# Kernel optimization log

Hardware: AMD Instinct MI355X
Metric: run time of the kernel (lower is better)

Reference implementation:

```python
import jax, jax.numpy as jnp
import numpy as np

C = 64        # channels
D = 64        # dense grid side at tensor_stride 1
N = 100000    # active voxels


def _conv3d(x, w, stride, pad):
    # x: (D,D,D,Cin), w: (kd,kh,kw,Cin,Cout) -> (D',D',D',Cout)
    return jax.lax.conv_general_dilated(
        x[None], w, window_strides=(stride,) * 3, padding=pad,
        dimension_numbers=('NDHWC', 'DHWIO', 'NDHWC'))[0]


def _sconv(x, w, b, mask, stride=1, pad='SAME'):
    # Minkowski sparse conv == dense conv on zero-filled grid, restricted to
    # the active output sites (bias only added at active sites).
    return (_conv3d(x, w, stride, pad) + b) * mask


def _forward(coords, coords_ds, feats_c1, feats_ref, w_fuse, b_fuse, w_down, b_down,
             w_conv2, b_conv2, w_p00, b_p00, w_p01, b_p01, w_p10, b_p10,
             w_p11, b_p11, w_p12, b_p12):
    dt = feats_c1.dtype
    Dh = D // 2
    ci, cj, ck = coords[:, 0], coords[:, 1], coords[:, 2]
    di, dj, dk = coords_ds[:, 0], coords_ds[:, 1], coords_ds[:, 2]
    mask = jnp.zeros((D, D, D, 1), dt).at[ci, cj, ck, 0].set(1.0)
    mask_ds = jnp.zeros((Dh, Dh, Dh, 1), dt).at[di, dj, dk, 0].set(1.0)
    fused = jnp.concatenate([feats_c1, feats_ref], axis=1)            # (N, 2C)
    x = jnp.zeros((D, D, D, 2 * C), dt).at[ci, cj, ck].set(fused)
    x = jax.nn.relu(_sconv(x, w_fuse, b_fuse, mask))                  # conv_fuse, k=3 s=1
    x = jax.nn.relu(_sconv(x, w_down, b_down, mask_ds, stride=2, pad='VALID'))  # conv_down1, k=2 s=2
    x = _sconv(x, w_conv2, b_conv2, mask_ds)                          # conv_2, no relu
    for i in range(w_p00.shape[0]):                                   # InceptionResNet x3
        p0 = jax.nn.relu(_sconv(x, w_p00[i], b_p00[i], mask_ds))      # k3 C->C/4
        p0 = _sconv(p0, w_p01[i], b_p01[i], mask_ds)                  # k3 C/4->C/2
        p1 = jax.nn.relu(_sconv(x, w_p10[i], b_p10[i], mask_ds))      # k1 C->C/4
        p1 = jax.nn.relu(_sconv(p1, w_p11[i], b_p11[i], mask_ds))     # k3 C/4->C/4
        p1 = _sconv(p1, w_p12[i], b_p12[i], mask_ds)                  # k1 C/4->C/2
        x = jnp.concatenate([p0, p1], axis=-1) + x                    # cat + residual
    return x[di, dj, dk]                                              # (M, C) sparse output feats


def setup_inputs() -> dict:
    rng = np.random.default_rng(0)
    flat = rng.choice(D ** 3, size=N, replace=False)                  # unique occupied voxels
    coords = np.stack(np.unravel_index(flat, (D, D, D)), axis=1).astype(np.int32)
    coords_ds = np.unique(coords // 2, axis=0).astype(np.int32)       # stride-2 active set
    key = jax.random.key(0)
    ks = iter(jax.random.split(key, 40))

    def W(shape, fan_in):
        return jax.random.normal(next(ks), shape, jnp.float32) / np.float32(np.sqrt(fan_in))

    def B(shape):
        return jax.random.normal(next(ks), shape, jnp.float32) * 0.01

    L = 3  # res blocks
    return dict(
        coords=jnp.asarray(coords), coords_ds=jnp.asarray(coords_ds),
        feats_c1=jax.random.normal(next(ks), (N, C), jnp.float32),
        feats_ref=jax.random.normal(next(ks), (N, C), jnp.float32),
        w_fuse=W((3, 3, 3, 2 * C, C), 27 * 2 * C), b_fuse=B((C,)),
        w_down=W((2, 2, 2, C, C), 8 * C), b_down=B((C,)),
        w_conv2=W((3, 3, 3, C, C), 27 * C), b_conv2=B((C,)),
        w_p00=W((L, 3, 3, 3, C, C // 4), 27 * C), b_p00=B((L, C // 4)),
        w_p01=W((L, 3, 3, 3, C // 4, C // 2), 27 * C // 4), b_p01=B((L, C // 2)),
        w_p10=W((L, 1, 1, 1, C, C // 4), C), b_p10=B((L, C // 4)),
        w_p11=W((L, 3, 3, 3, C // 4, C // 4), 27 * C // 4), b_p11=B((L, C // 4)),
        w_p12=W((L, 1, 1, 1, C // 4, C // 2), C // 4), b_p12=B((L, C // 2)),
    )


def reference(coords, coords_ds, feats_c1, feats_ref, w_fuse, b_fuse, w_down, b_down,
              w_conv2, b_conv2, w_p00, b_p00, w_p01, b_p01, w_p10, b_p10,
              w_p11, b_p11, w_p12, b_p12):
    return _forward(coords, coords_ds, feats_c1, feats_ref, w_fuse, b_fuse, w_down,
                    b_down, w_conv2, b_conv2, w_p00, b_p00, w_p01, b_p01, w_p10,
                    b_p10, w_p11, b_p11, w_p12, b_p12)
```

## Files before the change

### kernel.cpp

```cpp
#include <hip/hip_runtime.h>

#define GD 64
#define GDS 32

typedef _Float16 f16;
typedef __attribute__((ext_vector_type(8))) _Float16 f16x8;
typedef __attribute__((ext_vector_type(4))) float f32x4;

#define GLOAD_LDS16(SRC, DST)                                                        \
    __builtin_amdgcn_global_load_lds(                                                \
        (const __attribute__((address_space(1))) unsigned int*)(const void*)(SRC),   \
        (__attribute__((address_space(3))) unsigned int*)(void*)(DST), 16, 0, 0)

__global__ __launch_bounds__(256) void init_pack_kernel(
    int* __restrict__ idx_grid, unsigned char* __restrict__ ds_mask, f16* __restrict__ zrow,
    f16* __restrict__ f1z, const float* __restrict__ wf, const float* __restrict__ wd,
    const float* __restrict__ wc2, const float* __restrict__ wp00, const float* __restrict__ wp01,
    const float* __restrict__ wp10, const float* __restrict__ wp11, const float* __restrict__ wp12,
    const float* __restrict__ bp00, const float* __restrict__ bp01, const float* __restrict__ bp10,
    const float* __restrict__ bp11, int L, f16* __restrict__ wc1, f16* __restrict__ wdnh,
    f16* __restrict__ wc2h, f16* __restrict__ wfA, f16* __restrict__ wfB, f16* __restrict__ w12h,
    float* __restrict__ bA, float* __restrict__ bB) {
    int i0 = blockIdx.x * 256 + threadIdx.x;
    if (i0 < GD * GD * GD) idx_grid[i0] = -1;
    if (i0 < GDS * GDS * GDS) ds_mask[i0] = 0;
    if (i0 < 128) zrow[i0] = (f16)0.f;
    if (i0 < 64) f1z[i0] = (f16)0.f;

    int i = i0;
    int n;
    n = 27 * 8192;
    if (i < n) {
        int tap = i >> 13, oc = (i >> 7) & 63, ic = i & 127;
        wc1[i] = (f16)wf[(tap * 128 + ic) * 64 + oc];
        return;
    }
    i -= n;
    n = 8 * 4096;
    if (i < n) {
        int t = i >> 12, oc = (i >> 6) & 63, ic = i & 63;
        wdnh[i] = (f16)wd[(t * 64 + ic) * 64 + oc];
        return;
    }
    i -= n;
    n = 27 * 4096;
    if (i < n) {
        int tap = i >> 12, oc = (i >> 6) & 63, ic = i & 63;
        wc2h[i] = (f16)wc2[(tap * 64 + ic) * 64 + oc];
        return;
    }
    i -= n;
    n = L * 27 * 2048;
    if (i < n) {
        int l = i / (27 * 2048), r = i - l * 27 * 2048;
        int tap = r >> 11, oc = (r >> 6) & 31, ic = r & 63;
        float v = 0.f;
        if (oc < 16) v = wp00[(((size_t)l * 27 + tap) * 64 + ic) * 16 + oc];
        else if (tap == 13) v = wp10[((size_t)l * 64 + ic) * 16 + (oc - 16)];
        wfA[i] = (f16)v;
        return;
    }
    i -= n;
    n = L * 27 * 1536;
    if (i < n) {
        int l = i / (27 * 1536), r = i - l * 27 * 1536;
        int tap = r / 1536, q = r - tap * 1536;
        int oc = q >> 5, ic = q & 31;
        float v = 0.f;
        if (oc < 32) {
            if (ic < 16) v = wp01[(((size_t)l * 27 + tap) * 16 + ic) * 32 + oc];
        } else {
            if (ic >= 16) v = wp11[(((size_t)l * 27 + tap) * 16 + (ic - 16)) * 16 + (oc - 32)];
        }
        wfB[i] = (f16)v;
        return;
    }
    i -= n;
    n = L * 512;
    if (i < n) {
        int l = i >> 9, q = i & 511, oc = q >> 4, ic = q & 15;
        w12h[i] = (f16)wp12[((size_t)l * 16 + ic) * 32 + oc];
        return;
    }
    i -= n;
    n = L * 32;
    if (i < n) {
        int l = i >> 5, oc = i & 31;
        bA[i] = (oc < 16) ? bp00[l * 16 + oc] : bp10[l * 16 + oc - 16];
        return;
    }
    i -= n;
    n = L * 48;
    if (i < n) {
        int l = i / 48, c = i - l * 48;
        bB[i] = (c < 32) ? bp01[l * 32 + c] : bp11[l * 16 + (c - 32)];
    }
}

__global__ __launch_bounds__(256) void scatter_kernel(const int* __restrict__ coords, int N,
                                                      const int* __restrict__ coords_ds, int M,
                                                      int* __restrict__ idx_grid,
                                                      unsigned char* __restrict__ ds_mask) {
    int i = blockIdx.x * 256 + threadIdx.x;
    if (i < N) {
        int a = coords[i * 3], b = coords[i * 3 + 1], c = coords[i * 3 + 2];
        idx_grid[(a * GD + b) * GD + c] = i;
    }
    if (i < M) {
        int a = coords_ds[i * 3], b = coords_ds[i * 3 + 1], c = coords_ds[i * 3 + 2];
        ds_mask[(a * GDS + b) * GDS + c] = 1;
    }
}

__global__ __launch_bounds__(256) void count_kernel(const int* __restrict__ idx_grid,
                                                    int* __restrict__ cnt) {
    __shared__ int c;
    if (threadIdx.x == 0) c = 0;
    __syncthreads();
    int s = blockIdx.x * 256 + threadIdx.x;
    bool act = idx_grid[s] >= 0;
    unsigned long long m = __ballot(act);
    if ((threadIdx.x & 63) == 0) atomicAdd(&c, __popcll(m));
    __syncthreads();
    if (threadIdx.x == 0) cnt[blockIdx.x] = c;
}

__global__ __launch_bounds__(1024) void prefix_kernel(const int* __restrict__ cnt,
                                                      int* __restrict__ off) {
    __shared__ int s[1024];
    int t = threadIdx.x;
    int v0 = cnt[t];
    s[t] = v0;
    __syncthreads();
    for (int d = 1; d < 1024; d <<= 1) {
        int v = 0;
        if (t >= d) v = s[t - d];
        __syncthreads();
        s[t] += v;
        __syncthreads();
    }
    off[t] = s[t] - v0;
}

__global__ __launch_bounds__(256) void emit_kernel(int* __restrict__ idx_grid,
                                                   const int* __restrict__ off,
                                                   int* __restrict__ sites,
                                                   int* __restrict__ perm) {
    int tid = threadIdx.x, bid = blockIdx.x;
    int s = bid * 256 + tid;
    int orig = idx_grid[s];
    bool act = orig >= 0;
    unsigned long long m = __ballot(act);
    int lane = tid & 63, wv = tid >> 6;
    __shared__ int wcnt[4];
    if (lane == 0) wcnt[wv] = __popcll(m);
    __syncthreads();
    int base = off[bid];
    for (int w = 0; w < wv; ++w) base += wcnt[w];
    int rank = __popcll(m & ((1ull << lane) - 1ull));
    if (act) {
        int q = base + rank;
        sites[q] = s;
        perm[q] = orig;
        idx_grid[s] = q;
    }
}

__global__ __launch_bounds__(256) void fusef_kernel(const float* __restrict__ fc1,
                                                    const float* __restrict__ fref,
                                                    const int* __restrict__ perm, int N,
                                                    f16* __restrict__ feats) {
    int i = blockIdx.x * 256 + threadIdx.x;
    if (i < (N + 1) * 128) {
        int q = i >> 7, c = i & 127;
        float v = 0.f;
        if (q < N) {
            int p = perm[q];
            v = (c < 64) ? fc1[p * 64 + c] : fref[p * 64 + c - 64];
        }
        feats[i] = (f16)v;
    }
}

__global__ __launch_bounds__(512) void conv1_pipe(const int* __restrict__ sites,
                                                  const int* __restrict__ idx_grid, int N,
                                                  const f16* __restrict__ featsB,
                                                  const f16* __restrict__ wc1,
                                                  const float* __restrict__ bias,
                                                  f16* __restrict__ out ) {
    __shared__ f16 xb[2][64 * 128];
    __shared__ f16 wb[2][64 * 128];
    __shared__ int nbr[64 * 27];
    const int tid = threadIdx.x;
    const int nwg = gridDim.x, orig = blockIdx.x;
    const int qq = nwg >> 3, rr2 = nwg & 7;
    const int xcd = orig & 7, sub = orig >> 3;
    const int wg = (xcd < rr2 ? xcd * (qq + 1) : rr2 * (qq + 1) + (xcd - rr2) * qq) + sub;
    const int q0 = wg * 64;

    for (int t = tid; t < 64 * 27; t += 512) {
        int p = t / 27, tap = t - p * 27;
        int q = q0 + p, nb = N;
        if (q < N) {
            int s = sites[q];
            int i = (s >> 12) + tap / 9 - 1;
            int j = ((s >> 6) & 63) + (tap / 3) % 3 - 1;
            int k = (s & 63) + tap % 3 - 1;
            if ((unsigned)i < 64u && (unsigned)j < 64u && (unsigned)k < 64u) {
                int r = idx_grid[(i << 12) + (j << 6) + k];
                if (r >= 0) nb = r;
            }
        }
        nbr[t] = nb;
    }
    __syncthreads();

    const int lane = tid & 63, wid = tid >> 6;
    const int l16 = lane & 15, lq = lane >> 4;
    const int grp = wid >> 2, w4 = wid & 3;
    const int m0 = (w4 >> 1) * 32, n0 = (w4 & 1) * 32;

    auto STAGE = [&](int tap, int buf) {
#pragma unroll
        for (int r = 0; r < 2; ++r) {
            int slot = r * 512 + tid;
            int row = slot >> 4, cl = slot & 15;
            int c = cl ^ (row & 15);
            const f16* src = featsB + (size_t)nbr[row * 27 + tap] * 128 + c * 8;
            GLOAD_LDS16(src, &xb[buf][0] + (size_t)(r * 512 + (tid & ~63)) * 8);
        }
#pragma unroll
        for (int r = 0; r < 2; ++r) {
            int slot = r * 512 + tid;
            int row = slot >> 4, cl = slot & 15;
            int c = cl ^ (row & 15);
            const f16* src = wc1 + (size_t)((tap * 64 + row) * 128 + c * 8);
            GLOAD_LDS16(src, &wb[buf][0] + (size_t)(r * 512 + (tid & ~63)) * 8);
        }
    };

    f32x4 acc[2][2] = {};
    STAGE(0, 0);
    STAGE(1, 1);
    for (int tap = 0; tap < 27; ++tap) {
        if (tap < 26) {
            asm volatile("s_waitcnt vmcnt(4)" ::: "memory");
        } else {
            asm volatile("s_waitcnt vmcnt(0)" ::: "memory");
        }
        __builtin_amdgcn_sched_barrier(0);
        __builtin_amdgcn_s_barrier();

        if (grp == (tap & 1)) {
            const f16* xp = &xb[tap & 1][0];
            const f16* wp = &wb[tap & 1][0];
            f16x8 a[2][4], b[2][4];
#pragma unroll
            for (int mi = 0; mi < 2; ++mi) {
                int row = m0 + mi * 16 + l16;
#pragma unroll
                for (int ks = 0; ks < 4; ++ks)
                    a[mi][ks] = *(const f16x8*)(xp + (size_t)row * 128 +
                                                (size_t)((((ks * 4 + lq) ^ l16)) * 8));
            }
#pragma unroll
            for (int ni = 0; ni < 2; ++ni) {
                int col = n0 + ni * 16 + l16;
#pragma unroll
                for (int ks = 0; ks < 4; ++ks)
                    b[ni][ks] = *(const f16x8*)(wp + (size_t)col * 128 +
                                                (size_t)((((ks * 4 + lq) ^ l16)) * 8));
            }
#pragma unroll
            for (int mi = 0; mi < 2; ++mi)
#pragma unroll
                for (int ni = 0; ni < 2; ++ni)
#pragma unroll
                    for (int ks = 0; ks < 4; ++ks)
                        acc[mi][ni] = __builtin_amdgcn_mfma_f32_16x16x32_f16(a[mi][ks], b[ni][ks],
                                                                             acc[mi][ni], 0, 0, 0);
        }
        asm volatile("s_waitcnt lgkmcnt(0)" ::: "memory");
        __builtin_amdgcn_sched_barrier(0);
        __builtin_amdgcn_s_barrier();
        if (tap + 2 < 27) STAGE(tap + 2, tap & 1);
    }

    float* red = (float*)&xb[0][0];
    if (grp == 1) {
#pragma unroll
        for (int mi = 0; mi < 2; ++mi)
#pragma unroll
            for (int ni = 0; ni < 2; ++ni)
#pragma unroll
                for (int j = 0; j < 4; ++j)
                    red[(m0 + mi * 16 + lq * 4 + j) * 65 + n0 + ni * 16 + l16] = acc[mi][ni][j];
    }
    __syncthreads();
    if (grp == 0) {
#pragma unroll
        for (int ni = 0; ni < 2; ++ni) {
            int col = n0 + ni * 16 + l16;
            float bv = bias[col];
#pragma unroll
            for (int mi = 0; mi < 2; ++mi) {
#pragma unroll
                for (int j = 0; j < 4; ++j) {
                    int row = m0 + mi * 16 + lq * 4 + j;
                    int q = q0 + row;
                    if (q < N) {
                        float v = acc[mi][ni][j] + red[row * 65 + col] + bv;
                        out[(size_t)q * 64 + col] = (f16)(v > 0.f ? v : 0.f);
                    }
                }
            }
        }
    }
}

__global__ __launch_bounds__(512) void down_mfma(const f16* __restrict__ feats1h, int N,
                                                 const int* __restrict__ idx_grid,
                                                 const f16* __restrict__ wdn,
                                                 const float* __restrict__ bias,
                                                 const unsigned char* __restrict__ mask,
                                                 f16* __restrict__ out ) {
    __shared__ f16 xs[2][128 * 64];
    __shared__ f16 wl[2][512 * 8];
    __shared__ int nbr[128 * 8];
    const int tid = threadIdx.x;
    const int s0 = blockIdx.x * 128;
    for (int t = tid; t < 128 * 8; t += 512) {
        int sl = t >> 3, tp = t & 7;
        int s = s0 + sl;
        int i = s >> 10, j = (s >> 5) & 31, k = s & 31;
        int ci = 2 * i + (tp >> 2), cj = 2 * j + ((tp >> 1) & 1), ck = 2 * k + (tp & 1);
        int r = idx_grid[(ci * GD + cj) * GD + ck];
        nbr[t] = (r >= 0) ? r : N;
    }
    __syncthreads();
    auto STAGEX = [&](int tp, int buf) {
#pragma unroll
        for (int rr = 0; rr < 2; ++rr) {
            int slot = rr * 512 + tid;
            int row = slot >> 3, cl = slot & 7;
            int c = cl ^ (row & 7);
            const f16* src = feats1h + (size_t)nbr[row * 8 + tp] * 64 + c * 8;
            GLOAD_LDS16(src, &xs[buf][0] + (size_t)(rr * 512 + (tid & ~63)) * 8);
        }
    };
    auto STAGEW = [&](int tp, int buf) {
        int row = tid >> 3, cl = tid & 7;
        int c = cl ^ (row & 7);
        const f16* src = wdn + (size_t)((tp * 64 + row) * 64 + c * 8);
        GLOAD_LDS16(src, &wl[buf][0] + (size_t)(tid & ~63) * 8);
    };
    const int lane = tid & 63, wid = tid >> 6;
    const int l16 = lane & 15, lq = lane >> 4;
    const int wm = wid >> 1, wn = wid & 1;
    const int m0 = wm * 32, n0 = wn * 32;
    f32x4 acc[2][2] = {};
    STAGEX(0, 0);
    STAGEW(0, 0);
    STAGEX(1, 1);
    STAGEW(1, 1);
    for (int tp = 0; tp < 8; ++tp) {
        if (tp < 7) {
            asm volatile("s_waitcnt vmcnt(3)" ::: "memory");
        } else {
            asm volatile("s_waitcnt vmcnt(0)" ::: "memory");
        }
        __builtin_amdgcn_sched_barrier(0);
        __builtin_amdgcn_s_barrier();
        const f16* xbp = &xs[tp & 1][0];
        const f16* wbp = &wl[tp & 1][0];
        f16x8 a[2][2], bfr[2][2];
#pragma unroll
        for (int mi = 0; mi < 2; ++mi) {
            int row = m0 + mi * 16 + l16;
#pragma unroll
            for (int ks = 0; ks < 2; ++ks) {
                int ch = ks * 4 + lq;
                a[mi][ks] = *(const f16x8*)(xbp + (size_t)row * 64 + (ch ^ (row & 7)) * 8);
            }
        }
#pragma unroll
        for (int ni = 0; ni < 2; ++ni) {
            int col = n0 + ni * 16 + l16;
#pragma unroll
            for (int ks = 0; ks < 2; ++ks) {
                int ch = ks * 4 + lq;
                bfr[ni][ks] = *(const f16x8*)(wbp + (size_t)col * 64 + (ch ^ (col & 7)) * 8);
            }
        }
#pragma unroll
        for (int mi = 0; mi < 2; ++mi)
#pragma unroll
            for (int ni = 0; ni < 2; ++ni)
#pragma unroll
                for (int ks = 0; ks < 2; ++ks)
                    acc[mi][ni] = __builtin_amdgcn_mfma_f32_16x16x32_f16(a[mi][ks], bfr[ni][ks],
                                                                         acc[mi][ni], 0, 0, 0);
        asm volatile("s_waitcnt lgkmcnt(0)" ::: "memory");
        __builtin_amdgcn_sched_barrier(0);
        __builtin_amdgcn_s_barrier();
        if (tp + 2 < 8) {
            STAGEX(tp + 2, tp & 1);
            STAGEW(tp + 2, tp & 1);
        }
    }
#pragma unroll
    for (int mi = 0; mi < 2; ++mi) {
        int m = m0 + mi * 16 + lq * 4;
        int site = s0 + m;
        unsigned mword = *(const unsigned*)(mask + site);
#pragma unroll
        for (int ni = 0; ni < 2; ++ni) {
            int col = n0 + ni * 16 + l16;
            float bv = bias[col];
#pragma unroll
            for (int j = 0; j < 4; ++j) {
                float v = 0.f;
                if ((mword >> (8 * j)) & 255) {
                    v = acc[mi][ni][j] + bv;
                    v = v > 0.f ? v : 0.f;
                }
                out[(size_t)(site + j) * 64 + col] = (f16)v;
            }
        }
    }
}

template <int CIN, int COUT, int NW, int RELUFROM>
__global__ __launch_bounds__(512) void dconv_kernel(const f16* __restrict__ x,
                                                    const f16* __restrict__ wp,
                                                    const float* __restrict__ bias,
                                                    const unsigned char* __restrict__ mask,
                                                    const f16* __restrict__ zrow,
                                                    f16* __restrict__ out, int ostr) {
    constexpr int NCH = CIN / 8;
    constexpr int PSLOT = 34 * NCH;
    constexpr int STOT = 18 * PSLOT;
    constexpr int RNDS = (STOT + 511) / 512;
    constexpr int MW = 8 / NW;
    constexpr int WM = 128 / MW, WN = COUT / NW;
    constexpr int FM = WM / 16, FN = WN / 16, KS = CIN / 32;
    constexpr int WSLOTS = COUT * NCH;
    __shared__ f16 xs[RNDS * 512 * 8];
    __shared__ f16 wl[2][512 * 8];

    const int tid = threadIdx.x;
    const int bid = blockIdx.x;
    const int i0 = bid >> 3, j0 = (bid & 7) * 4;

    for (int rr = 0; rr < RNDS; ++rr) {
        int slot = rr * 512 + tid;
        int p = slot / PSLOT;
        int rem = slot - p * PSLOT;
        int r = rem / NCH;
        int cl = rem - r * NCH;
        int c = cl ^ (r & (NCH - 1));
        int gi = i0 + p / 6 - 1, gj = j0 + p % 6 - 1, gk = r - 1;
        bool ok = (slot < STOT) && ((unsigned)gi < 32u) && ((unsigned)gj < 32u) &&
                  ((unsigned)gk < 32u);
        const f16* src = ok ? (x + (size_t)(((gi * 32 + gj) * 32 + gk) * CIN + c * 8)) : zrow;
        f16* dst = xs + (size_t)(rr * 512 + (tid & ~63)) * 8;
        GLOAD_LDS16(src, dst);
    }
    auto STAGEW = [&](int tap, int buf) {
        int row = tid / NCH, cl = tid % NCH;
        int c = cl ^ (row & (NCH - 1));
        const f16* src = (tid < WSLOTS) ? (wp + (size_t)((tap * COUT + row) * CIN + c * 8)) : wp;
        GLOAD_LDS16(src, &wl[buf][0] + (size_t)(tid & ~63) * 8);
    };
    STAGEW(0, 0);
    STAGEW(1, 1);

    const int lane = tid & 63, wid = tid >> 6;
    const int l16 = lane & 15, lq = lane >> 4;
    const int wm = wid / NW, wn = wid - wm * NW;
    const int m0 = wm * WM, n0 = wn * WN;

    f32x4 acc[FM][FN] = {};

    for (int tap = 0; tap < 27; ++tap) {
        if (tap < 26) {
            asm volatile("s_waitcnt vmcnt(1)" ::: "memory");
        } else {
            asm volatile("s_waitcnt vmcnt(0)" ::: "memory");
        }
        __builtin_amdgcn_sched_barrier(0);
        __builtin_amdgcn_s_barrier();

        int di = tap / 9 - 1, dj = (tap / 3) % 3 - 1, dk = tap % 3 - 1;
        const f16* wbp = &wl[tap & 1][0];
        f16x8 a[FM][KS], bfr[FN][KS];
#pragma unroll
        for (int mi = 0; mi < FM; ++mi) {
            int m = m0 + mi * 16 + l16;
            int pj = m >> 5, k = m & 31;
            int p = (di + 1) * 6 + (pj + dj + 1);
            int r = k + dk + 1;
#pragma unroll
            for (int ks = 0; ks < KS; ++ks) {
                int ch = ks * 4 + lq;
                a[mi][ks] =
                    *(const f16x8*)(xs + (size_t)(p * PSLOT + r * NCH + (ch ^ (r & (NCH - 1)))) * 8);
            }
        }
#pragma unroll
        for (int ni = 0; ni < FN; ++ni) {
            int col = n0 + ni * 16 + l16;
#pragma unroll
            for (int ks = 0; ks < KS; ++ks) {
                int ch = ks * 4 + lq;
                bfr[ni][ks] =
                    *(const f16x8*)(wbp + (size_t)(col * NCH + (ch ^ (col & (NCH - 1)))) * 8);
            }
        }
#pragma unroll
        for (int mi = 0; mi < FM; ++mi)
#pragma unroll
            for (int ni = 0; ni < FN; ++ni)
#pragma unroll
                for (int ks = 0; ks < KS; ++ks)
                    acc[mi][ni] = __builtin_amdgcn_mfma_f32_16x16x32_f16(a[mi][ks], bfr[ni][ks],
                                                                         acc[mi][ni], 0, 0, 0);
        asm volatile("s_waitcnt lgkmcnt(0)" ::: "memory");
        __builtin_amdgcn_sched_barrier(0);
        __builtin_amdgcn_s_barrier();
        if (tap + 2 < 27) STAGEW(tap + 2, tap & 1);
    }

#pragma unroll
    for (int mi = 0; mi < FM; ++mi) {
        int m = m0 + mi * 16 + lq * 4;
        int pj = m >> 5, k = m & 31;
        int gsite = ((i0 * 32) + (j0 + pj)) * 32 + k;
        unsigned mword = *(const unsigned*)(mask + gsite);
#pragma unroll
        for (int ni = 0; ni < FN; ++ni) {
            int col = n0 + ni * 16 + l16;
            float bv = bias[col];
#pragma unroll
            for (int j = 0; j < 4; ++j) {
                float v = 0.f;
                if ((mword >> (8 * j)) & 255) {
                    v = acc[mi][ni][j] + bv;
                    if (col >= RELUFROM) v = v > 0.f ? v : 0.f;
                }
                out[(size_t)(gsite + j) * ostr + col] = (f16)v;
            }
        }
    }
}

template <typename OUTT>
__global__ __launch_bounds__(256) void tail_kernel(const f16* __restrict__ ph,
                                                   const f16* __restrict__ xh,
                                                   const f16* __restrict__ w12,
                                                   const float* __restrict__ b12,
                                                   const unsigned char* __restrict__ mask,
                                                   OUTT* __restrict__ y ) {
    __shared__ float ws[512];
    __shared__ float bs[32];
    int tid = threadIdx.x;
    ws[tid] = (float)w12[tid];
    ws[tid + 256] = (float)w12[tid + 256];
    if (tid < 32) bs[tid] = b12[tid];
    __syncthreads();
    int g = tid >> 6, lane = tid & 63;
    int site = blockIdx.x * 64 + lane;
    const f16x8* pr = (const f16x8*)(ph + (size_t)site * 64);
    const f16x8* xr = (const f16x8*)(xh + (size_t)site * 64);
    float yv[16];
    int col0;
    if (g < 2) {
        col0 = g * 16;
        f16x8 p0 = pr[g * 2], p1 = pr[g * 2 + 1];
        f16x8 x0 = xr[g * 2], x1 = xr[g * 2 + 1];
#pragma unroll
        for (int j = 0; j < 8; ++j) {
            yv[j] = (float)p0[j] + (float)x0[j];
            yv[8 + j] = (float)p1[j] + (float)x1[j];
        }
    } else {
        int oc0 = (g - 2) * 16;
        col0 = 32 + oc0;
        f16x8 u0 = pr[4], u1 = pr[5];
        float u[16];
#pragma unroll
        for (int j = 0; j < 8; ++j) {
            u[j] = (float)u0[j];
            u[8 + j] = (float)u1[j];
        }
        f16x8 x0 = xr[4 + (g - 2) * 2], x1 = xr[5 + (g - 2) * 2];
        bool mk = mask[site] != 0;
#pragma unroll
        for (int oc = 0; oc < 16; ++oc) {
            float s = 0.f;
#pragma unroll
            for (int ic = 0; ic < 16; ++ic) s += u[ic] * ws[(oc0 + oc) * 16 + ic];
            float p1v = mk ? (s + bs[oc0 + oc]) : 0.f;
            yv[oc] = p1v + (float)((oc < 8) ? x0[oc] : x1[oc - 8]);
        }
    }
#pragma unroll
    for (int j = 0; j < 16; ++j) y[(size_t)site * 64 + col0 + j] = (OUTT)yv[j];
}

__global__ __launch_bounds__(256) void gather_kernel(const float* __restrict__ x,
                                                     const int* __restrict__ coords_ds, int M,
                                                     float* __restrict__ out) {
    int i = blockIdx.x * 256 + threadIdx.x;
    if (i < M * 64) {
        int m = i >> 6, oc = i & 63;
        int a = coords_ds[m * 3], b = coords_ds[m * 3 + 1], c = coords_ds[m * 3 + 2];
        out[i] = x[((size_t)((a * GDS + b) * GDS + c) << 6) + oc];
    }
}

extern "C" void kernel_launch(void* const* d_in, const int* in_sizes, int n_in,
                              void* d_out, int out_size, void* d_ws, size_t ws_size,
                              hipStream_t stream) {
    const int* coords = (const int*)d_in[0];
    const int* coords_ds = (const int*)d_in[1];
    const float* fc1 = (const float*)d_in[2];
    const float* fref = (const float*)d_in[3];
    const float* w_fuse = (const float*)d_in[4];
    const float* b_fuse = (const float*)d_in[5];
    const float* w_down = (const float*)d_in[6];
    const float* b_down = (const float*)d_in[7];
    const float* w_conv2 = (const float*)d_in[8];
    const float* b_conv2 = (const float*)d_in[9];
    const float* w_p00 = (const float*)d_in[10];
    const float* b_p00 = (const float*)d_in[11];
    const float* w_p01 = (const float*)d_in[12];
    const float* b_p01 = (const float*)d_in[13];
    const float* w_p10 = (const float*)d_in[14];
    const float* b_p10 = (const float*)d_in[15];
    const float* w_p11 = (const float*)d_in[16];
    const float* b_p11 = (const float*)d_in[17];
    const float* w_p12 = (const float*)d_in[18];
    const float* b_p12 = (const float*)d_in[19];

    const int N = in_sizes[0] / 3;
    const int M = in_sizes[1] / 3;
    const int L = in_sizes[10] / (27 * 64 * 16);
    const int NSITES = GDS * GDS * GDS;

    size_t off = 0;
    auto alloc = [&](size_t bytes) {
        void* p = (char*)d_ws + off;
        off += (bytes + 255) & ~(size_t)255;
        return p;
    };
    int* idx_grid = (int*)alloc((size_t)GD * GD * GD * 4);
    unsigned char* ds_mask = (unsigned char*)alloc(NSITES);
    f16* zrow = (f16*)alloc(256);
    int* chunk_cnt = (int*)alloc(1024 * 4);
    int* chunk_off = (int*)alloc(1024 * 4);
    int* sites = (int*)alloc((size_t)N * 4);
    int* perm = (int*)alloc((size_t)N * 4);
    f16* featsB = (f16*)alloc((size_t)(N + 1) * 128 * 2);
    f16* feats1h = (f16*)alloc((size_t)(N + 1) * 64 * 2);
    f16* xdown = (f16*)alloc((size_t)NSITES * 64 * 2);
    f16* x0 = (f16*)alloc((size_t)NSITES * 64 * 2);
    f16* y1 = (f16*)alloc((size_t)NSITES * 64 * 2);
    f16* y2 = (f16*)alloc((size_t)NSITES * 64 * 2);
    f16* thh = (f16*)alloc((size_t)NSITES * 32 * 2);
    f16* ph = (f16*)alloc((size_t)NSITES * 64 * 2);
    float* xF = (float*)alloc((size_t)NSITES * 64 * 4);
    f16* wc1 = (f16*)alloc((size_t)27 * 8192 * 2);
    f16* wdnh = (f16*)alloc((size_t)8 * 4096 * 2);
    f16* wc2h = (f16*)alloc((size_t)27 * 4096 * 2);
    f16* wfA = (f16*)alloc((size_t)L * 27 * 2048 * 2);
    f16* wfB = (f16*)alloc((size_t)L * 27 * 1536 * 2);
    f16* w12h = (f16*)alloc((size_t)L * 512 * 2);
    float* bA = (float*)alloc((size_t)L * 32 * 4);
    float* bB = (float*)alloc((size_t)L * 48 * 4);
    (void)ws_size;

    float* out = (float*)d_out;
    (void)out_size;
    (void)n_in;

    {
        int tot = 27 * 8192 + 8 * 4096 + 27 * 4096 + L * 27 * 2048 + L * 27 * 1536 + L * 512 +
                  L * 32 + L * 48;
        if (tot < GD * GD * GD) tot = GD * GD * GD;
        init_pack_kernel<<<(tot + 255) / 256, 256, 0, stream>>>(
            idx_grid, ds_mask, zrow, feats1h + (size_t)N * 64, w_fuse, w_down, w_conv2, w_p00,
            w_p01, w_p10, w_p11, w_p12, b_p00, b_p01, b_p10, b_p11, L, wc1, wdnh, wc2h, wfA, wfB,
            w12h, bA, bB);
    }
    {
        int mx = N > M ? N : M;
        scatter_kernel<<<(mx + 255) / 256, 256, 0, stream>>>(coords, N, coords_ds, M, idx_grid,
                                                             ds_mask);
    }
    count_kernel<<<1024, 256, 0, stream>>>(idx_grid, chunk_cnt);
    prefix_kernel<<<1, 1024, 0, stream>>>(chunk_cnt, chunk_off);
    emit_kernel<<<1024, 256, 0, stream>>>(idx_grid, chunk_off, sites, perm);
    fusef_kernel<<<((N + 1) * 128 + 255) / 256, 256, 0, stream>>>(fc1, fref, perm, N, featsB);

    conv1_pipe<<<(N + 63) / 64, 512, 0, stream>>>(sites, idx_grid, N, featsB, wc1, b_fuse,
                                                  feats1h);
    down_mfma<<<NSITES / 128, 512, 0, stream>>>(feats1h, N, idx_grid, wdnh, b_down, ds_mask,
                                                xdown);
    dconv_kernel<64, 64, 2, 64>
        <<<256, 512, 0, stream>>>(xdown, wc2h, b_conv2, ds_mask, zrow, x0, 64);

    f16* x = x0;
    for (int l = 0; l < L; ++l) {
        dconv_kernel<64, 32, 2, 0>
            <<<256, 512, 0, stream>>>(x, wfA + (size_t)l * 27 * 2048, bA + l * 32, ds_mask, zrow,
                                      thh, 32);
        dconv_kernel<32, 48, 1, 32>
            <<<256, 512, 0, stream>>>(thh, wfB + (size_t)l * 27 * 1536, bB + l * 48, ds_mask, zrow,
                                      ph, 64);
        if (l < L - 1) {
            f16* yn = (l == 0) ? y1 : y2;
            tail_kernel<f16><<<NSITES / 64, 256, 0, stream>>>(ph, x, w12h + (size_t)l * 512,
                                                              b_p12 + l * 32, ds_mask, yn);
            x = yn;
        } else {
            tail_kernel<float><<<NSITES / 64, 256, 0, stream>>>(ph, x, w12h + (size_t)l * 512,
                                                                b_p12 + l * 32, ds_mask, xF);
        }
    }

    gather_kernel<<<(M * 64 + 255) / 256, 256, 0, stream>>>(xF, coords_ds, M, out);
}
```

Baseline: 274.3 us.

## Fuse second branch conv with residual tail and halve dconv tile size

```diff
diff --git a/kernel.cpp b/kernel.cpp
--- a/kernel.cpp
+++ b/kernel.cpp
@@ -431,7 +431,7 @@
 }
 
 template <int CIN, int COUT, int NW, int RELUFROM>
-__global__ __launch_bounds__(512) void dconv_kernel(const f16* __restrict__ x,
+__global__ __launch_bounds__(256) void dconv_kernel(const f16* __restrict__ x,
                                                     const f16* __restrict__ wp,
                                                     const float* __restrict__ bias,
                                                     const unsigned char* __restrict__ mask,
@@ -439,38 +439,43 @@
                                                     f16* __restrict__ out, int ostr) {
     constexpr int NCH = CIN / 8;
     constexpr int PSLOT = 34 * NCH;
-    constexpr int STOT = 18 * PSLOT;
-    constexpr int RNDS = (STOT + 511) / 512;
-    constexpr int MW = 8 / NW;
-    constexpr int WM = 128 / MW, WN = COUT / NW;
+    constexpr int STOT = 12 * PSLOT;
+    constexpr int RNDS = (STOT + 255) / 256;
+    constexpr int MW = 4 / NW;
+    constexpr int WM = 64 / MW, WN = COUT / NW;
     constexpr int FM = WM / 16, FN = WN / 16, KS = CIN / 32;
     constexpr int WSLOTS = COUT * NCH;
-    __shared__ f16 xs[RNDS * 512 * 8];
-    __shared__ f16 wl[2][512 * 8];
+    constexpr int WR = (WSLOTS + 255) / 256;
+    __shared__ f16 xs[RNDS * 256 * 8];
+    __shared__ f16 wl[2][WR * 256 * 8];
 
     const int tid = threadIdx.x;
     const int bid = blockIdx.x;
-    const int i0 = bid >> 3, j0 = (bid & 7) * 4;
+    const int i0 = bid >> 4, j0 = (bid & 15) * 2;
 
     for (int rr = 0; rr < RNDS; ++rr) {
-        int slot = rr * 512 + tid;
+        int slot = rr * 256 + tid;
         int p = slot / PSLOT;
         int rem = slot - p * PSLOT;
         int r = rem / NCH;
         int cl = rem - r * NCH;
         int c = cl ^ (r & (NCH - 1));
-        int gi = i0 + p / 6 - 1, gj = j0 + p % 6 - 1, gk = r - 1;
+        int gi = i0 + p / 4 - 1, gj = j0 + (p & 3) - 1, gk = r - 1;
         bool ok = (slot < STOT) && ((unsigned)gi < 32u) && ((unsigned)gj < 32u) &&
                   ((unsigned)gk < 32u);
         const f16* src = ok ? (x + (size_t)(((gi * 32 + gj) * 32 + gk) * CIN + c * 8)) : zrow;
-        f16* dst = xs + (size_t)(rr * 512 + (tid & ~63)) * 8;
-        GLOAD_LDS16(src, dst);
+        GLOAD_LDS16(src, xs + (size_t)(rr * 256 + (tid & ~63)) * 8);
     }
     auto STAGEW = [&](int tap, int buf) {
-        int row = tid / NCH, cl = tid % NCH;
-        int c = cl ^ (row & (NCH - 1));
-        const f16* src = (tid < WSLOTS) ? (wp + (size_t)((tap * COUT + row) * CIN + c * 8)) : wp;
-        GLOAD_LDS16(src, &wl[buf][0] + (size_t)(tid & ~63) * 8);
+#pragma unroll
+        for (int r = 0; r < WR; ++r) {
+            int slot = r * 256 + tid;
+            int row = slot / NCH, cl = slot % NCH;
+            int c = cl ^ (row & (NCH - 1));
+            const f16* src =
+                (slot < WSLOTS) ? (wp + (size_t)((tap * COUT + row) * CIN + c * 8)) : wp;
+            GLOAD_LDS16(src, &wl[buf][0] + (size_t)(r * 256 + (tid & ~63)) * 8);
+        }
     };
     STAGEW(0, 0);
     STAGEW(1, 1);
@@ -484,7 +489,7 @@
 
     for (int tap = 0; tap < 27; ++tap) {
         if (tap < 26) {
-            asm volatile("s_waitcnt vmcnt(1)" ::: "memory");
+            asm volatile("s_waitcnt vmcnt(%0)" ::"i"(WR) : "memory");
         } else {
             asm volatile("s_waitcnt vmcnt(0)" ::: "memory");
         }
@@ -498,7 +503,7 @@
         for (int mi = 0; mi < FM; ++mi) {
             int m = m0 + mi * 16 + l16;
             int pj = m >> 5, k = m & 31;
-            int p = (di + 1) * 6 + (pj + dj + 1);
+            int p = (di + 1) * 4 + (pj + dj + 1);
             int r = k + dk + 1;
 #pragma unroll
             for (int ks = 0; ks < KS; ++ks) {
@@ -555,57 +560,133 @@
 }
 
 template <typename OUTT>
-__global__ __launch_bounds__(256) void tail_kernel(const f16* __restrict__ ph,
-                                                   const f16* __restrict__ xh,
-                                                   const f16* __restrict__ w12,
-                                                   const float* __restrict__ b12,
-                                                   const unsigned char* __restrict__ mask,
-                                                   OUTT* __restrict__ y ) {
-    __shared__ float ws[512];
-    __shared__ float bs[32];
-    int tid = threadIdx.x;
-    ws[tid] = (float)w12[tid];
-    ws[tid + 256] = (float)w12[tid + 256];
-    if (tid < 32) bs[tid] = b12[tid];
-    __syncthreads();
-    int g = tid >> 6, lane = tid & 63;
-    int site = blockIdx.x * 64 + lane;
-    const f16x8* pr = (const f16x8*)(ph + (size_t)site * 64);
-    const f16x8* xr = (const f16x8*)(xh + (size_t)site * 64);
-    float yv[16];
-    int col0;
-    if (g < 2) {
-        col0 = g * 16;
-        f16x8 p0 = pr[g * 2], p1 = pr[g * 2 + 1];
-        f16x8 x0 = xr[g * 2], x1 = xr[g * 2 + 1];
-#pragma unroll
-        for (int j = 0; j < 8; ++j) {
-            yv[j] = (float)p0[j] + (float)x0[j];
-            yv[8 + j] = (float)p1[j] + (float)x1[j];
-        }
-    } else {
-        int oc0 = (g - 2) * 16;
-        col0 = 32 + oc0;
-        f16x8 u0 = pr[4], u1 = pr[5];
-        float u[16];
-#pragma unroll
-        for (int j = 0; j < 8; ++j) {
-            u[j] = (float)u0[j];
-            u[8 + j] = (float)u1[j];
-        }
-        f16x8 x0 = xr[4 + (g - 2) * 2], x1 = xr[5 + (g - 2) * 2];
-        bool mk = mask[site] != 0;
-#pragma unroll
-        for (int oc = 0; oc < 16; ++oc) {
-            float s = 0.f;
-#pragma unroll
-            for (int ic = 0; ic < 16; ++ic) s += u[ic] * ws[(oc0 + oc) * 16 + ic];
-            float p1v = mk ? (s + bs[oc0 + oc]) : 0.f;
-            yv[oc] = p1v + (float)((oc < 8) ? x0[oc] : x1[oc - 8]);
-        }
-    }
-#pragma unroll
-    for (int j = 0; j < 16; ++j) y[(size_t)site * 64 + col0 + j] = (OUTT)yv[j];
+__global__ __launch_bounds__(256) void fb_tail_kernel(const f16* __restrict__ x,
+                                                      const f16* __restrict__ wp,
+                                                      const float* __restrict__ bias,
+                                                      const unsigned char* __restrict__ mask,
+                                                      const f16* __restrict__ zrow,
+                                                      const f16* __restrict__ xh,
+                                                      const f16* __restrict__ w12,
+                                                      const float* __restrict__ b12,
+                                                      OUTT* __restrict__ y ) {
+    constexpr int NCH = 4;
+    constexpr int PSLOT = 34 * NCH;
+    constexpr int STOT = 12 * PSLOT;
+    constexpr int RNDS = (STOT + 255) / 256;
+    __shared__ f16 xs[RNDS * 256 * 8];
+    __shared__ f16 wl[2][256 * 8];
+    __shared__ float ws12[512];
+    __shared__ float bs12[32];
+    __shared__ float u1s[64 * 17];
+
+    const int tid = threadIdx.x;
+    const int bid = blockIdx.x;
+    const int i0 = bid >> 4, j0 = (bid & 15) * 2;
+
+    for (int rr = 0; rr < RNDS; ++rr) {
+        int slot = rr * 256 + tid;
+        int p = slot / PSLOT;
+        int rem = slot - p * PSLOT;
+        int r = rem / NCH;
+        int cl = rem - r * NCH;
+        int c = cl ^ (r & 3);
+        int gi = i0 + p / 4 - 1, gj = j0 + (p & 3) - 1, gk = r - 1;
+        bool ok = (slot < STOT) && ((unsigned)gi < 32u) && ((unsigned)gj < 32u) &&
+                  ((unsigned)gk < 32u);
+        const f16* src = ok ? (x + (size_t)(((gi * 32 + gj) * 32 + gk) * 32 + c * 8)) : zrow;
+        GLOAD_LDS16(src, xs + (size_t)(rr * 256 + (tid & ~63)) * 8);
+    }
+    auto STAGEW = [&](int tap, int buf) {
+        int row = tid >> 2, cl = tid & 3;
+        int c = cl ^ (row & 3);
+        const f16* src = (tid < 192) ? (wp + (size_t)((tap * 48 + row) * 32 + c * 8)) : wp;
+        GLOAD_LDS16(src, &wl[buf][0] + (size_t)(tid & ~63) * 8);
+    };
+    STAGEW(0, 0);
+    STAGEW(1, 1);
+    ws12[tid] = (float)w12[tid];
+    ws12[tid + 256] = (float)w12[tid + 256];
+    if (tid < 32) bs12[tid] = b12[tid];
+
+    const int lane = tid & 63, wid = tid >> 6;
+    const int l16 = lane & 15, lq = lane >> 4;
+    const int m0 = wid * 16;
+
+    f32x4 acc[3] = {};
+
+    for (int tap = 0; tap < 27; ++tap) {
+        if (tap < 26) {
+            asm volatile("s_waitcnt vmcnt(1)" ::: "memory");
+        } else {
+            asm volatile("s_waitcnt vmcnt(0)" ::: "memory");
+        }
+        __builtin_amdgcn_sched_barrier(0);
+        __builtin_amdgcn_s_barrier();
+
+        int di = tap / 9 - 1, dj = (tap / 3) % 3 - 1, dk = tap % 3 - 1;
+        const f16* wbp = &wl[tap & 1][0];
+        int m = m0 + l16;
+        int pj = m >> 5, k = m & 31;
+        int p = (di + 1) * 4 + (pj + dj + 1);
+        int r = k + dk + 1;
+        f16x8 a = *(const f16x8*)(xs + (size_t)(p * PSLOT + r * NCH + (lq ^ (r & 3))) * 8);
+        f16x8 bfr[3];
+#pragma unroll
+        for (int ni = 0; ni < 3; ++ni) {
+            int col = ni * 16 + l16;
+            bfr[ni] = *(const f16x8*)(wbp + (size_t)(col * NCH + (lq ^ (col & 3))) * 8);
+        }
+#pragma unroll
+        for (int ni = 0; ni < 3; ++ni)
+            acc[ni] = __builtin_amdgcn_mfma_f32_16x16x32_f16(a, bfr[ni], acc[ni], 0, 0, 0);
+        asm volatile("s_waitcnt lgkmcnt(0)" ::: "memory");
+        __builtin_amdgcn_sched_barrier(0);
+        __builtin_amdgcn_s_barrier();
+        if (tap + 2 < 27) STAGEW(tap + 2, tap & 1);
+    }
+
+    {
+        int mrow = m0 + lq * 4;
+        int pj = mrow >> 5, k = mrow & 31;
+        int gsite = ((i0 * 32) + (j0 + pj)) * 32 + k;
+        unsigned mword = *(const unsigned*)(mask + gsite);
+#pragma unroll
+        for (int j = 0; j < 4; ++j) {
+            float u = 0.f;
+            if ((mword >> (8 * j)) & 255) {
+                u = acc[2][j] + bias[32 + l16];
+                u = u > 0.f ? u : 0.f;
+            }
+            u1s[(mrow + j) * 17 + l16] = u;
+        }
+        asm volatile("s_waitcnt lgkmcnt(0)" ::: "memory");
+        __builtin_amdgcn_sched_barrier(0);
+        float b0 = bias[l16], b1 = bias[16 + l16];
+        float tb0 = bs12[l16], tb1 = bs12[16 + l16];
+#pragma unroll
+        for (int j = 0; j < 4; ++j) {
+            int mr = mrow + j;
+            int site = gsite + j;
+            bool mk = ((mword >> (8 * j)) & 255) != 0;
+            const f16* xr = xh + (size_t)site * 64;
+            OUTT* yr = y + (size_t)site * 64;
+            float p0a = mk ? (acc[0][j] + b0) : 0.f;
+            float p0b = mk ? (acc[1][j] + b1) : 0.f;
+            yr[l16] = (OUTT)(p0a + (float)xr[l16]);
+            yr[16 + l16] = (OUTT)(p0b + (float)xr[16 + l16]);
+            float s0 = 0.f, s1 = 0.f;
+#pragma unroll
+            for (int ic = 0; ic < 16; ++ic) {
+                float u = u1s[mr * 17 + ic];
+                s0 += u * ws12[l16 * 16 + ic];
+                s1 += u * ws12[(16 + l16) * 16 + ic];
+            }
+            float p1a = mk ? (s0 + tb0) : 0.f;
+            float p1b = mk ? (s1 + tb1) : 0.f;
+            yr[32 + l16] = (OUTT)(p1a + (float)xr[32 + l16]);
+            yr[48 + l16] = (OUTT)(p1b + (float)xr[48 + l16]);
+        }
+    }
 }
 
 __global__ __launch_bounds__(256) void gather_kernel(const float* __restrict__ x,
@@ -668,7 +749,6 @@
     f16* y1 = (f16*)alloc((size_t)NSITES * 64 * 2);
     f16* y2 = (f16*)alloc((size_t)NSITES * 64 * 2);
     f16* thh = (f16*)alloc((size_t)NSITES * 32 * 2);
-    f16* ph = (f16*)alloc((size_t)NSITES * 64 * 2);
     float* xF = (float*)alloc((size_t)NSITES * 64 * 4);
     f16* wc1 = (f16*)alloc((size_t)27 * 8192 * 2);
     f16* wdnh = (f16*)alloc((size_t)8 * 4096 * 2);
@@ -708,24 +788,23 @@
     down_mfma<<<NSITES / 128, 512, 0, stream>>>(feats1h, N, idx_grid, wdnh, b_down, ds_mask,
                                                 xdown);
     dconv_kernel<64, 64, 2, 64>
-        <<<256, 512, 0, stream>>>(xdown, wc2h, b_conv2, ds_mask, zrow, x0, 64);
+        <<<512, 256, 0, stream>>>(xdown, wc2h, b_conv2, ds_mask, zrow, x0, 64);
 
     f16* x = x0;
     for (int l = 0; l < L; ++l) {
         dconv_kernel<64, 32, 2, 0>
-            <<<256, 512, 0, stream>>>(x, wfA + (size_t)l * 27 * 2048, bA + l * 32, ds_mask, zrow,
+            <<<512, 256, 0, stream>>>(x, wfA + (size_t)l * 27 * 2048, bA + l * 32, ds_mask, zrow,
                                       thh, 32);
-        dconv_kernel<32, 48, 1, 32>
-            <<<256, 512, 0, stream>>>(thh, wfB + (size_t)l * 27 * 1536, bB + l * 48, ds_mask, zrow,
-                                      ph, 64);
         if (l < L - 1) {
             f16* yn = (l == 0) ? y1 : y2;
-            tail_kernel<f16><<<NSITES / 64, 256, 0, stream>>>(ph, x, w12h + (size_t)l * 512,
-                                                              b_p12 + l * 32, ds_mask, yn);
+            fb_tail_kernel<f16><<<512, 256, 0, stream>>>(
+                thh, wfB + (size_t)l * 27 * 1536, bB + l * 48, ds_mask, zrow, x,
+                w12h + (size_t)l * 512, b_p12 + l * 32, yn);
             x = yn;
         } else {
-            tail_kernel<float><<<NSITES / 64, 256, 0, stream>>>(ph, x, w12h + (size_t)l * 512,
-                                                                b_p12 + l * 32, ds_mask, xF);
+            fb_tail_kernel<float><<<512, 256, 0, stream>>>(
+                thh, wfB + (size_t)l * 27 * 1536, bB + l * 48, ds_mask, zrow, x,
+                w12h + (size_t)l * 512, b_p12 + l * 32, xF);
         }
     }
 
```

Measured after the change: 274.5 us (median of 2 runs). No clear change (+0.1%).
